# Optimization experiments

Measured on AMD Instinct MI355X. Metric: run time of the kernel, lower is better.

Reference implementation:

```python
import jax, jax.numpy as jnp
import numpy as np

# Production-scale dims inferred from graph_construct / coord_cuda:
# coord_cuda: [batch, total_len, mat_h*mat_w, edge_num, 2]
B, T, C, H, W, K = 4, 8, 32, 40, 40, 9
EPS = 1e-8


def setup_inputs() -> dict:
    key = jax.random.key(0)
    sim_feat = jax.random.normal(key, (B, T, C, H, W), dtype=jnp.float32)
    return {"sim_feat": sim_feat}


def reference(sim_feat):
    """Motion-graph construction: similarity matrix between consecutive
    frames' node features, kNN edge selection (top edge_num), per-node
    edge weight normalization, and coordinate-displacement node init."""
    b, t, c, h, w = sim_feat.shape
    hw = h * w
    # [B, T, hw, c] node features
    feat = sim_feat.reshape(b, t, c, hw).transpose(0, 1, 3, 2)
    # cosine-style normalization for the similarity matrix
    fn = feat * jax.lax.rsqrt(jnp.sum(feat * feat, axis=-1, keepdims=True) + EPS)
    # build_similarity_matrix ('forward'): frame t nodes vs frame t+1 nodes
    # sim: [B, T-1, hw, hw] -- dominant, memory-bound intermediate
    sim = jnp.einsum('btic,btjc->btij', fn[:, :-1], fn[:, 1:])
    # build_graph_edge: top edge_num candidate edges per source node
    wgt, idx = jax.lax.top_k(sim, K)          # [B, T-1, hw, K]
    # edge_normalize: weights sum to 1 over the K edges of each node
    wgt = wgt / (jnp.sum(wgt, axis=-1, keepdims=True) + EPS)
    # target node 2D coords (y, x) via gather on flat index
    ty = idx // w
    tx = idx % w
    # source node coords (motion_node_indices analogue)
    src = jnp.arange(hw, dtype=idx.dtype)
    sy = (src // w)[None, None, :, None]
    sx = (src % w)[None, None, :, None]
    # node_init = target coord - source coord (motion displacement), [B,T-1,hw,K,2]
    node_init = jnp.stack([ty - sy, tx - sx], axis=-1)
    return wgt, idx, node_init
```

## Files before the change

### kernel.cpp

```cpp
#include <hip/hip_runtime.h>
#include <math.h>

#define BD   4
#define TD   8
#define CD   32
#define WD   40
#define KD   9
#define HWD  1600
#define TM1  7
#define NPAIR (BD * TM1)
#define OUTK ((size_t)NPAIR * HWD * KD)
#define CL   6
#define NEX  12

#define FNW_OFF   0
#define TRAW_OFF  3276800
#define RND_OFF   9830400

typedef __attribute__((ext_vector_type(8))) short short8;
typedef __attribute__((ext_vector_type(4))) float f32x4;

__device__ __forceinline__ uint f2bf(float f) {
    uint u = __float_as_uint(f);
    return (u + 0x7FFFu + ((u >> 16) & 1u)) >> 16;
}

__global__ __launch_bounds__(256)
void prep_kernel(const float* __restrict__ x, uint* __restrict__ fnw,
                 float* __restrict__ traw, double* __restrict__ rnd)
{
    const int gid  = blockIdx.x * 256 + threadIdx.x;
    const int q    = gid & 3;
    const int idx  = gid >> 2;
    const int bt   = idx / HWD;
    const int node = idx - bt * HWD;

    const float* src = x + (size_t)bt * CD * HWD + node;
    float v[8];
    float ssq = 0.f;
    double ssd = 0.0;
#pragma unroll
    for (int cc = 0; cc < 8; ++cc) {
        const float a = src[(size_t)(q * 8 + cc) * HWD];
        v[cc] = a;
        ssq += a * a;
        ssd = fma((double)a, (double)a, ssd);
    }
    ssq += __shfl_xor(ssq, 1);  ssq += __shfl_xor(ssq, 2);
    ssd += __shfl_xor(ssd, 1);  ssd += __shfl_xor(ssd, 2);

    const float rn = 1.0f / sqrtf(ssq + 1e-8f);
    if (q == 0) rnd[(size_t)bt * HWD + node] = 1.0 / sqrt(ssd + 1e-8);

    uint* dstb = fnw + (size_t)(bt * HWD + node) * 16 + q * 4;
    const uint w0 = f2bf(v[0]*rn) | (f2bf(v[1]*rn) << 16);
    const uint w1 = f2bf(v[2]*rn) | (f2bf(v[3]*rn) << 16);
    const uint w2 = f2bf(v[4]*rn) | (f2bf(v[5]*rn) << 16);
    const uint w3 = f2bf(v[6]*rn) | (f2bf(v[7]*rn) << 16);
    *(uint4*)dstb = make_uint4(w0, w1, w2, w3);

    float* dstr = traw + (size_t)(bt * HWD + node) * 32 + q * 8;
    ((float4*)dstr)[0] = make_float4(v[0], v[1], v[2], v[3]);
    ((float4*)dstr)[1] = make_float4(v[4], v[5], v[6], v[7]);
}

__global__ __launch_bounds__(256)
void topk_kernel(const uint* __restrict__ fnw, const float* __restrict__ traw,
                 const double* __restrict__ rnd, float* __restrict__ out)
{
    const int tid  = threadIdx.x;
    const int lane = tid & 63;
    const int wid  = tid >> 6;
    const int li   = lane & 15;
    const int gr   = lane >> 4;

    const int bid  = blockIdx.x;
    const int xcd  = bid & 7;
    const int kk   = bid >> 3;
    const int work = (xcd < 4) ? (xcd * 88 + kk) : (352 + (xcd - 4) * 87 + kk);
    const int f    = work / 25;
    const int ibk  = work - f * 25;
    const int b    = f / TM1;
    const int t    = f - b * TM1;
    const int bt0  = b * TD + t;
    const int bt1  = bt0 + 1;
    const int i    = ibk * 64 + wid * 16 + li;

    const uint* fA = fnw + (size_t)bt0 * HWD * 16;
    const uint* fB = fnw + (size_t)bt1 * HWD * 16;

    const short8 bF = *(const short8*)(fA + (size_t)i * 16 + gr * 4);

    uint C[4][CL];
#pragma unroll
    for (int r = 0; r < 4; ++r)
#pragma unroll
        for (int k = 0; k < CL; ++k) C[r][k] = 0u;

    int jr[4];
#pragma unroll
    for (int r = 0; r < 4; ++r) jr[r] = 2047 - 4 * gr - r;

    const f32x4 one4 = {1.f, 1.f, 1.f, 1.f};

#define LDT(dst, s) dst = *(const short8*)(fB + (size_t)((s) * 16 + li) * 16 + gr * 4)

#define INSTILE(acc) do {                                              \
    _Pragma("unroll")                                                  \
    for (int r = 0; r < 4; ++r) {                                      \
        int ub = __float_as_int((acc)[r]);                             \
        ub = ub < 0 ? 0 : ub;                                          \
        uint u = ((uint)ub & 0xFFFFF800u) | (uint)jr[r];               \
        uint tv = u;                                                   \
        _Pragma("unroll")                                              \
        for (int k = 0; k < CL; ++k) {                                 \
            const uint lo = min(C[r][k], tv);                          \
            C[r][k] = max(C[r][k], tv);                                \
            tv = lo;                                                   \
        }                                                              \
        jr[r] -= 16;                                                   \
    }                                                                  \
} while (0)

    short8 a0, a1, a2, a3;
    LDT(a0, 0); LDT(a1, 1); LDT(a2, 2); LDT(a3, 3);

    for (int sb = 0; sb < 96; sb += 4) {
        f32x4 acc;
        acc = __builtin_amdgcn_mfma_f32_16x16x32_bf16(a0, bF, one4, 0, 0, 0);
        LDT(a0, sb + 4);
        INSTILE(acc);
        acc = __builtin_amdgcn_mfma_f32_16x16x32_bf16(a1, bF, one4, 0, 0, 0);
        LDT(a1, sb + 5);
        INSTILE(acc);
        acc = __builtin_amdgcn_mfma_f32_16x16x32_bf16(a2, bF, one4, 0, 0, 0);
        LDT(a2, sb + 6);
        INSTILE(acc);
        acc = __builtin_amdgcn_mfma_f32_16x16x32_bf16(a3, bF, one4, 0, 0, 0);
        LDT(a3, sb + 7);
        INSTILE(acc);
    }
    {
        f32x4 acc;
        acc = __builtin_amdgcn_mfma_f32_16x16x32_bf16(a0, bF, one4, 0, 0, 0);
        INSTILE(acc);
        acc = __builtin_amdgcn_mfma_f32_16x16x32_bf16(a1, bF, one4, 0, 0, 0);
        INSTILE(acc);
        acc = __builtin_amdgcn_mfma_f32_16x16x32_bf16(a2, bF, one4, 0, 0, 0);
        INSTILE(acc);
        acc = __builtin_amdgcn_mfma_f32_16x16x32_bf16(a3, bF, one4, 0, 0, 0);
        INSTILE(acc);
    }
#undef LDT
#undef INSTILE

    const float* tA = traw + (size_t)bt0 * HWD * 32 + (size_t)i * 32;
    float arf[CD];
#pragma unroll
    for (int q = 0; q < 8; ++q) {
        const float4 r4 = ((const float4*)tA)[q];
        arf[4*q+0] = r4.x; arf[4*q+1] = r4.y; arf[4*q+2] = r4.z; arf[4*q+3] = r4.w;
    }
    const double rna = rnd[(size_t)bt0 * HWD + i];
    const float*  trB = traw + (size_t)bt1 * HWD * 32;
    const double* rnB = rnd + (size_t)bt1 * HWD;

    double fv[KD]; int fi[KD];
#pragma unroll
    for (int k = 0; k < KD; ++k) { fv[k] = -1.0e300; fi[k] = 0; }

    for (int rd = 0; rd < NEX; ++rd) {
        const uint m = max(max(C[0][0], C[1][0]), max(C[2][0], C[3][0]));
#pragma unroll
        for (int r = 0; r < 4; ++r) {
            const bool e = (C[r][0] == m);
#pragma unroll
            for (int k = 0; k < CL - 1; ++k) C[r][k] = e ? C[r][k + 1] : C[r][k];
            C[r][CL - 1] = e ? 0u : C[r][CL - 1];
        }
        const int j = 2047 - (int)(m & 2047u);
        const float4* rb = (const float4*)(trB + (size_t)j * 32);
        double dot = 0.0;
#pragma unroll
        for (int q = 0; q < 8; ++q) {
            const float4 r4 = rb[q];
            dot = fma((double)arf[4*q+0], (double)r4.x, dot);
            dot = fma((double)arf[4*q+1], (double)r4.y, dot);
            dot = fma((double)arf[4*q+2], (double)r4.z, dot);
            dot = fma((double)arf[4*q+3], (double)r4.w, dot);
        }
        const double val = dot * rna * rnB[j];
        if (val > fv[KD - 1]) {
            bool bg[KD];
#pragma unroll
            for (int k = 0; k < KD; ++k) bg[k] = val > fv[k];
#pragma unroll
            for (int k = KD - 1; k >= 1; --k) {
                fv[k] = bg[k - 1] ? fv[k - 1] : (bg[k] ? val : fv[k]);
                fi[k] = bg[k - 1] ? fi[k - 1] : (bg[k] ? j : fi[k]);
            }
            if (bg[0]) { fv[0] = val; fi[0] = j; }
        }
    }

    double w9v[KD]; int w9j[KD];
#pragma unroll
    for (int rd = 0; rd < KD; ++rd) {
        double hv = fv[0]; int hj = fi[0];
        {
            const double ov = __shfl_xor(hv, 16); const int oj = __shfl_xor(hj, 16);
            const bool tk = (ov > hv) || (ov == hv && oj < hj);
            hv = tk ? ov : hv; hj = tk ? oj : hj;
        }
        {
            const double ov = __shfl_xor(hv, 32); const int oj = __shfl_xor(hj, 32);
            const bool tk = (ov > hv) || (ov == hv && oj < hj);
            hv = tk ? ov : hv; hj = tk ? oj : hj;
        }
        w9v[rd] = hv; w9j[rd] = hj;
        const bool win = (fi[0] == hj);
#pragma unroll
        for (int k = 0; k < KD - 1; ++k) {
            fv[k] = win ? fv[k + 1] : fv[k];
            fi[k] = win ? fi[k + 1] : fi[k];
        }
        if (win) fv[KD - 1] = -1.0e300;
    }

    double wsum = 0.0;
#pragma unroll
    for (int k = 0; k < KD; ++k) wsum += w9v[k];
    const double winv = 1.0 / (wsum + 1e-8);

    const size_t base = ((size_t)f * HWD + i) * KD;
    const int sy = i / WD, sx = i - sy * WD;
    if (gr == 0) {
#pragma unroll
        for (int k = 0; k < KD; ++k) out[base + k] = (float)(w9v[k] * winv);
    } else if (gr == 1) {
#pragma unroll
        for (int k = 0; k < KD; ++k) out[OUTK + base + k] = (float)w9j[k];
    } else if (gr == 2) {
#pragma unroll
        for (int k = 0; k < KD; ++k) {
            const int j = w9j[k];
            out[2 * OUTK + (base + k) * 2 + 0] = (float)(j / WD - sy);
        }
    } else {
#pragma unroll
        for (int k = 0; k < KD; ++k) {
            const int j = w9j[k];
            out[2 * OUTK + (base + k) * 2 + 1] = (float)(j - (j / WD) * WD - sx);
        }
    }
}

extern "C" void kernel_launch(void* const* d_in, const int* in_sizes, int n_in,
                              void* d_out, int out_size, void* d_ws, size_t ws_size,
                              hipStream_t stream)
{
    const float* x = (const float*)d_in[0];
    uint*   fnw  = (uint*)((char*)d_ws + FNW_OFF);
    float*  traw = (float*)((char*)d_ws + TRAW_OFF);
    double* rnd  = (double*)((char*)d_ws + RND_OFF);
    float*  out  = (float*)d_out;

    prep_kernel<<<dim3((TD * BD * HWD * 4) / 256), 256, 0, stream>>>(x, fnw, traw, rnd);
    topk_kernel<<<dim3(NPAIR * 25), 256, 0, stream>>>(fnw, traw, rnd, out);
}
```

Before: 130.1 us.

## Split candidate scan across two wave halves and merge shortlists via LDS

Each block now covers 32 source nodes instead of 64, with two waves per node group scanning disjoint halves of the 1600 target nodes. Each half extracts its own top-12 candidate list, and the second half passes its list through shared memory to the first, which merges the two sorted lists before the exact double-precision rescoring. This doubles the grid and shortens each wave's serial MFMA-plus-insertion chain, at the cost of a block barrier, idle waves during the rescoring phase, and more total candidate extraction work. The fp64 dot product is also split into four independent accumulators to shorten its dependency chain, and launch bounds now request occupancy 4.

```diff
diff --git a/kernel.cpp b/kernel.cpp
--- a/kernel.cpp
+++ b/kernel.cpp
@@ -64,27 +64,31 @@
     ((float4*)dstr)[1] = make_float4(v[4], v[5], v[6], v[7]);
 }
 
-__global__ __launch_bounds__(256)
+__global__ __launch_bounds__(256, 4)
 void topk_kernel(const uint* __restrict__ fnw, const float* __restrict__ traw,
                  const double* __restrict__ rnd, float* __restrict__ out)
 {
+    __shared__ uint s_ext[2][64][NEX];
+
     const int tid  = threadIdx.x;
     const int lane = tid & 63;
     const int wid  = tid >> 6;
     const int li   = lane & 15;
     const int gr   = lane >> 4;
+    const int iq   = wid & 1;
+    const int half = wid >> 1;
 
     const int bid  = blockIdx.x;
     const int xcd  = bid & 7;
     const int kk   = bid >> 3;
-    const int work = (xcd < 4) ? (xcd * 88 + kk) : (352 + (xcd - 4) * 87 + kk);
-    const int f    = work / 25;
-    const int ibk  = work - f * 25;
+    const int work = xcd * 175 + kk;
+    const int f    = work / 50;
+    const int rem  = work - f * 50;
     const int b    = f / TM1;
     const int t    = f - b * TM1;
     const int bt0  = b * TD + t;
     const int bt1  = bt0 + 1;
-    const int i    = ibk * 64 + wid * 16 + li;
+    const int i    = rem * 32 + iq * 16 + li;
 
     const uint* fA = fnw + (size_t)bt0 * HWD * 16;
     const uint* fB = fnw + (size_t)bt1 * HWD * 16;
@@ -99,7 +103,7 @@
 
     int jr[4];
 #pragma unroll
-    for (int r = 0; r < 4; ++r) jr[r] = 2047 - 4 * gr - r;
+    for (int r = 0; r < 4; ++r) jr[r] = 2047 - half * 800 - 4 * gr - r;
 
     const f32x4 one4 = {1.f, 1.f, 1.f, 1.f};
 
@@ -122,10 +126,11 @@
     }                                                                  \
 } while (0)
 
+    const int s0 = half * 50;
     short8 a0, a1, a2, a3;
-    LDT(a0, 0); LDT(a1, 1); LDT(a2, 2); LDT(a3, 3);
-
-    for (int sb = 0; sb < 96; sb += 4) {
+    LDT(a0, s0); LDT(a1, s0 + 1); LDT(a2, s0 + 2); LDT(a3, s0 + 3);
+
+    for (int sb = s0; sb < s0 + 44; sb += 4) {
         f32x4 acc;
         acc = __builtin_amdgcn_mfma_f32_16x16x32_bf16(a0, bF, one4, 0, 0, 0);
         LDT(a0, sb + 4);
@@ -143,16 +148,50 @@
     {
         f32x4 acc;
         acc = __builtin_amdgcn_mfma_f32_16x16x32_bf16(a0, bF, one4, 0, 0, 0);
+        LDT(a0, s0 + 48);
         INSTILE(acc);
         acc = __builtin_amdgcn_mfma_f32_16x16x32_bf16(a1, bF, one4, 0, 0, 0);
+        LDT(a1, s0 + 49);
         INSTILE(acc);
         acc = __builtin_amdgcn_mfma_f32_16x16x32_bf16(a2, bF, one4, 0, 0, 0);
         INSTILE(acc);
         acc = __builtin_amdgcn_mfma_f32_16x16x32_bf16(a3, bF, one4, 0, 0, 0);
+        INSTILE(acc);
+        acc = __builtin_amdgcn_mfma_f32_16x16x32_bf16(a0, bF, one4, 0, 0, 0);
+        INSTILE(acc);
+        acc = __builtin_amdgcn_mfma_f32_16x16x32_bf16(a1, bF, one4, 0, 0, 0);
         INSTILE(acc);
     }
 #undef LDT
 #undef INSTILE
+
+    uint sA[NEX];
+#pragma unroll
+    for (int rd = 0; rd < NEX; ++rd) {
+        const uint m = max(max(C[0][0], C[1][0]), max(C[2][0], C[3][0]));
+#pragma unroll
+        for (int r = 0; r < 4; ++r) {
+            const bool e = (C[r][0] == m);
+#pragma unroll
+            for (int k = 0; k < CL - 1; ++k) C[r][k] = e ? C[r][k + 1] : C[r][k];
+            C[r][CL - 1] = e ? 0u : C[r][CL - 1];
+        }
+        sA[rd] = m;
+    }
+
+    if (half == 1) {
+#pragma unroll
+        for (int k = 0; k < NEX; ++k) s_ext[iq][lane][k] = sA[k];
+    }
+    __syncthreads();
+    if (half == 1) return;
+
+    uint sB[NEX];
+#pragma unroll
+    for (int q = 0; q < 3; ++q) {
+        const uint4 v4 = *(const uint4*)&s_ext[iq][lane][q * 4];
+        sB[q*4+0] = v4.x; sB[q*4+1] = v4.y; sB[q*4+2] = v4.z; sB[q*4+3] = v4.w;
+    }
 
     const float* tA = traw + (size_t)bt0 * HWD * 32 + (size_t)i * 32;
     float arf[CD];
@@ -170,26 +209,25 @@
     for (int k = 0; k < KD; ++k) { fv[k] = -1.0e300; fi[k] = 0; }
 
     for (int rd = 0; rd < NEX; ++rd) {
-        const uint m = max(max(C[0][0], C[1][0]), max(C[2][0], C[3][0]));
-#pragma unroll
-        for (int r = 0; r < 4; ++r) {
-            const bool e = (C[r][0] == m);
-#pragma unroll
-            for (int k = 0; k < CL - 1; ++k) C[r][k] = e ? C[r][k + 1] : C[r][k];
-            C[r][CL - 1] = e ? 0u : C[r][CL - 1];
+        const bool tAh = sA[0] > sB[0];
+        const uint m = tAh ? sA[0] : sB[0];
+#pragma unroll
+        for (int k = 0; k < NEX - 1; ++k) {
+            sA[k] = tAh ? sA[k + 1] : sA[k];
+            sB[k] = tAh ? sB[k] : sB[k + 1];
         }
         const int j = 2047 - (int)(m & 2047u);
         const float4* rb = (const float4*)(trB + (size_t)j * 32);
-        double dot = 0.0;
+        double d0 = 0.0, d1 = 0.0, d2 = 0.0, d3 = 0.0;
 #pragma unroll
         for (int q = 0; q < 8; ++q) {
             const float4 r4 = rb[q];
-            dot = fma((double)arf[4*q+0], (double)r4.x, dot);
-            dot = fma((double)arf[4*q+1], (double)r4.y, dot);
-            dot = fma((double)arf[4*q+2], (double)r4.z, dot);
-            dot = fma((double)arf[4*q+3], (double)r4.w, dot);
-        }
-        const double val = dot * rna * rnB[j];
+            d0 = fma((double)arf[4*q+0], (double)r4.x, d0);
+            d1 = fma((double)arf[4*q+1], (double)r4.y, d1);
+            d2 = fma((double)arf[4*q+2], (double)r4.z, d2);
+            d3 = fma((double)arf[4*q+3], (double)r4.w, d3);
+        }
+        const double val = ((d0 + d1) + (d2 + d3)) * rna * rnB[j];
         if (val > fv[KD - 1]) {
             bool bg[KD];
 #pragma unroll
@@ -266,5 +304,5 @@
     float*  out  = (float*)d_out;
 
     prep_kernel<<<dim3((TD * BD * HWD * 4) / 256), 256, 0, stream>>>(x, fnw, traw, rnd);
-    topk_kernel<<<dim3(NPAIR * 25), 256, 0, stream>>>(fnw, traw, rnd, out);
+    topk_kernel<<<dim3(NPAIR * 50), 256, 0, stream>>>(fnw, traw, rnd, out);
 }
```

Measured after the change: 150.1 us. +15.4%, slower.
